# Kernel tuning notes

Measured on AMD Instinct MI355X. Metric: run time of the kernel, lower is better.

The kernel has to match this reference:

```python
import jax, jax.numpy as jnp
import numpy as np
import math

N_HEAD = 16

def setup_inputs() -> dict:
    key = jax.random.key(0)
    k1, k2, k3, k4, k5 = jax.random.split(key, 5)
    B, T, C = 8, 1024, 1024
    scale = 0.02
    return {
        "x": jax.random.normal(k1, (B, T, C), dtype=jnp.float32),
        "w_attn": jax.random.normal(k2, (C, 3 * C), dtype=jnp.float32) * scale,
        "b_attn": jax.random.normal(k3, (3 * C,), dtype=jnp.float32) * scale,
        "w_proj": jax.random.normal(k4, (C, C), dtype=jnp.float32) * scale,
        "b_proj": jax.random.normal(k5, (C,), dtype=jnp.float32) * scale,
    }

def reference(x, w_attn, b_attn, w_proj, b_proj):
    B, T, C = x.shape
    H = N_HEAD
    hd = C // H
    # QKV projection: [B,T,3C]
    qkv = jnp.einsum("btc,cd->btd", x, w_attn) + b_attn
    q, k, v = jnp.split(qkv, 3, axis=-1)
    # [B,T,C] -> [B,H,T,hd]
    def heads(t):
        return t.reshape(B, T, H, hd).transpose(0, 2, 1, 3)
    q, k, v = heads(q), heads(k), heads(v)
    # scaled QK^T: [B,H,T,T]
    att = jnp.einsum("bhqd,bhkd->bhqk", q, k) * (1.0 / math.sqrt(hd))
    # causal mask (tril of block_size cropped to T)
    causal = jnp.tril(jnp.ones((T, T), dtype=bool))
    att = jnp.where(causal, att, jnp.float32(-jnp.inf))
    att = jax.nn.softmax(att, axis=-1)
    # attention-weighted values: [B,H,T,hd] -> [B,T,C]
    y = jnp.einsum("bhqk,bhkd->bhqd", att, v)
    y = y.transpose(0, 2, 1, 3).reshape(B, T, C)
    # output projection
    return jnp.einsum("btc,cd->btd", y, w_proj) + b_proj
```

## Files before the change

kernel.cpp:

```cpp
#include <hip/hip_runtime.h>

typedef __bf16 bf16x8 __attribute__((ext_vector_type(8)));
typedef float f32x4 __attribute__((ext_vector_type(4)));
typedef unsigned short u16;
typedef unsigned int u32;
typedef unsigned long long u64;

__device__ __forceinline__ u16 f2bf(float f) {
  u32 u = __builtin_bit_cast(u32, f);
  u32 r = (u + 0x7FFFu + ((u >> 16) & 1u)) >> 16;
  return (u16)r;
}

__device__ __forceinline__ void gload_lds16(const u16* g, u16* l) {
  __builtin_amdgcn_global_load_lds(
      (const __attribute__((address_space(1))) u32*)g,
      (__attribute__((address_space(3))) u32*)l, 16, 0, 0);
}

__global__ void cast_x_kernel(const float* __restrict__ in, u16* __restrict__ out, int n4) {
  int i = blockIdx.x * blockDim.x + threadIdx.x;
  if (i >= n4) return;
  float4 v = ((const float4*)in)[i];
  uint2 o;
  o.x = (u32)f2bf(v.x) | ((u32)f2bf(v.y) << 16);
  o.y = (u32)f2bf(v.z) | ((u32)f2bf(v.w) << 16);
  ((uint2*)out)[i] = o;
}

__global__ void transpose_cast_kernel(const float* __restrict__ in, u16* __restrict__ out,
                                      int K, int N) {
  __shared__ float tile[32][33];
  int n0 = blockIdx.x * 32, k0 = blockIdx.y * 32;
  int tx = threadIdx.x & 31, ty = threadIdx.x >> 5;
#pragma unroll
  for (int i = 0; i < 32; i += 8)
    tile[ty + i][tx] = in[(size_t)(k0 + ty + i) * N + n0 + tx];
  __syncthreads();
#pragma unroll
  for (int i = 0; i < 32; i += 8)
    out[(size_t)(n0 + ty + i) * K + k0 + tx] = f2bf(tile[tx][ty + i]);
}

__global__ __launch_bounds__(512, 2) void gemm256qk(
    const u16* __restrict__ A, const u16* __restrict__ Bt,
    const float* __restrict__ bias, u16* __restrict__ out_q,
    int M, int N, int K) {
  __shared__ alignas(16) u16 lds[2][2][256 * 64];
  const int tiles_n = N >> 8;
  const int bid = blockIdx.x;
  const int cpx = (int)gridDim.x >> 3;
  const int swz = (bid & 7) * cpx + (bid >> 3);
  const int tm = swz / tiles_n, tn = swz % tiles_n;
  const int tid = threadIdx.x, lane = tid & 63;
  const int w = tid >> 6, wm = w >> 2, wn = w & 3;
  const int lr = lane & 15, lg = lane >> 4;
  const int NT = K >> 6;

  f32x4 acc[2][2][4][2] = {};

  auto stage = [&](int t, int which) {
    const int isB = which & 1, half = which >> 1;
    const u16* mat = isB ? Bt : A;
    const int row0 = (isB ? tn : tm) * 256 + half * 128;
    u16* lbase = &lds[t & 1][isB][half * 8192];
#pragma unroll
    for (int j = 0; j < 2; ++j) {
      int c = tid + j * 512;
      int k8 = (c & 7) ^ ((c >> 3) & 7);
      int row = c >> 3;
      gload_lds16(mat + (size_t)(row0 + row) * K + t * 64 + k8 * 8, lbase + c * 8);
    }
  };
  auto rdA = [&](int cur, int mh, int m, int kk) -> bf16x8 {
    int row = mh * 128 + wm * 64 + m * 16 + lr;
    int e = (row * 64 + kk * 32 + lg * 8) ^ ((row & 7) << 3);
    return *(const bf16x8*)&lds[cur][0][e];
  };
  auto rdB = [&](int cur, int nh, int n, int kk) -> bf16x8 {
    int row = nh * 128 + wn * 32 + n * 16 + lr;
    int e = (row * 64 + kk * 32 + lg * 8) ^ ((row & 7) << 3);
    return *(const bf16x8*)&lds[cur][1][e];
  };

  stage(0, 0); stage(0, 1); stage(0, 2); stage(0, 3);
  stage(1, 0); stage(1, 1); stage(1, 2);
  asm volatile("s_waitcnt vmcnt(6)" ::: "memory");
  __builtin_amdgcn_s_barrier();

  bf16x8 af[4][2], b0[2][2], b1[2][2];
  for (int t = 0; t < NT; ++t) {
    const int cur = t & 1;
#pragma unroll
    for (int m = 0; m < 4; ++m)
#pragma unroll
      for (int kk = 0; kk < 2; ++kk) af[m][kk] = rdA(cur, 0, m, kk);
#pragma unroll
    for (int n = 0; n < 2; ++n)
#pragma unroll
      for (int kk = 0; kk < 2; ++kk) b0[n][kk] = rdB(cur, 0, n, kk);
    if (t + 1 < NT) stage(t + 1, 3);
    __builtin_amdgcn_s_barrier();
    asm volatile("s_waitcnt lgkmcnt(0)" ::: "memory");
    __builtin_amdgcn_s_setprio(1);
#pragma unroll
    for (int m = 0; m < 4; ++m)
#pragma unroll
      for (int n = 0; n < 2; ++n)
#pragma unroll
        for (int kk = 0; kk < 2; ++kk)
          acc[0][0][m][n] = __builtin_amdgcn_mfma_f32_16x16x32_bf16(b0[n][kk], af[m][kk], acc[0][0][m][n], 0, 0, 0);
    __builtin_amdgcn_s_setprio(0);
    __builtin_amdgcn_s_barrier();
#pragma unroll
    for (int n = 0; n < 2; ++n)
#pragma unroll
      for (int kk = 0; kk < 2; ++kk) b1[n][kk] = rdB(cur, 1, n, kk);
    if (t + 2 < NT) stage(t + 2, 0);
    __builtin_amdgcn_s_barrier();
    asm volatile("s_waitcnt lgkmcnt(0)" ::: "memory");
    __builtin_amdgcn_s_setprio(1);
#pragma unroll
    for (int m = 0; m < 4; ++m)
#pragma unroll
      for (int n = 0; n < 2; ++n)
#pragma unroll
        for (int kk = 0; kk < 2; ++kk)
          acc[0][1][m][n] = __builtin_amdgcn_mfma_f32_16x16x32_bf16(b1[n][kk], af[m][kk], acc[0][1][m][n], 0, 0, 0);
    __builtin_amdgcn_s_setprio(0);
    __builtin_amdgcn_s_barrier();
#pragma unroll
    for (int m = 0; m < 4; ++m)
#pragma unroll
      for (int kk = 0; kk < 2; ++kk) af[m][kk] = rdA(cur, 1, m, kk);
    if (t + 2 < NT) stage(t + 2, 1);
    __builtin_amdgcn_s_barrier();
    asm volatile("s_waitcnt lgkmcnt(0)" ::: "memory");
    __builtin_amdgcn_s_setprio(1);
#pragma unroll
    for (int m = 0; m < 4; ++m)
#pragma unroll
      for (int n = 0; n < 2; ++n)
#pragma unroll
        for (int kk = 0; kk < 2; ++kk)
          acc[1][0][m][n] = __builtin_amdgcn_mfma_f32_16x16x32_bf16(b0[n][kk], af[m][kk], acc[1][0][m][n], 0, 0, 0);
    __builtin_amdgcn_s_setprio(0);
    __builtin_amdgcn_s_barrier();
    if (t + 2 < NT) stage(t + 2, 2);
    __builtin_amdgcn_s_barrier();
    __builtin_amdgcn_s_setprio(1);
#pragma unroll
    for (int m = 0; m < 4; ++m)
#pragma unroll
      for (int n = 0; n < 2; ++n)
#pragma unroll
        for (int kk = 0; kk < 2; ++kk)
          acc[1][1][m][n] = __builtin_amdgcn_mfma_f32_16x16x32_bf16(b1[n][kk], af[m][kk], acc[1][1][m][n], 0, 0, 0);
    __builtin_amdgcn_s_setprio(0);
    if (t + 2 < NT) {
      asm volatile("s_waitcnt vmcnt(6)" ::: "memory");
    } else {
      asm volatile("s_waitcnt vmcnt(0)" ::: "memory");
    }
    __builtin_amdgcn_s_barrier();
  }

#pragma unroll
  for (int mh = 0; mh < 2; ++mh)
#pragma unroll
    for (int nh = 0; nh < 2; ++nh)
#pragma unroll
      for (int n = 0; n < 2; ++n) {
        int ncol = tn * 256 + nh * 128 + wn * 32 + n * 16 + lg * 4;
        float4 bv = *(const float4*)&bias[ncol];
        int which = ncol >> 10, c = ncol & 1023;
        int h = c >> 6, d = c & 63;
#pragma unroll
        for (int m = 0; m < 4; ++m) {
          int tok = tm * 256 + mh * 128 + wm * 64 + m * 16 + lr;
          int b = tok >> 10, t = tok & 1023;
          union { u16 s[4]; uint2 v; } pk;
          pk.s[0] = f2bf(acc[mh][nh][m][n][0] + bv.x);
          pk.s[1] = f2bf(acc[mh][nh][m][n][1] + bv.y);
          pk.s[2] = f2bf(acc[mh][nh][m][n][2] + bv.z);
          pk.s[3] = f2bf(acc[mh][nh][m][n][3] + bv.w);
          *(uint2*)&out_q[(size_t)which * 8388608 + ((((size_t)b * 16 + h) * 1024 + t) << 6) + d] = pk.v;
        }
      }
}

template <int MODE>
__global__ __launch_bounds__(256, 3) void gemm_bf16(
    const u16* __restrict__ A, const u16* __restrict__ Bt,
    const float* __restrict__ bias, u16* __restrict__ out_q,
    float* __restrict__ out_f, int M, int N, int K) {
  __shared__ alignas(16) u16 As[128 * 64];
  __shared__ alignas(16) u16 Bs[128 * 64];
  const int tiles_n = N >> 7;
  const int bid0 = blockIdx.x;
  const int cpx = (int)gridDim.x >> 3;
  const int swz = (bid0 & 7) * cpx + (bid0 >> 3);
  const int tm = swz / tiles_n;
  const int tn = swz % tiles_n;
  const int tid = threadIdx.x;
  const int wave = tid >> 6, lane = tid & 63;
  const int wr = (wave >> 1) * 64, wc = (wave & 1) * 64;
  const int lr = lane & 15, lg = lane >> 4;

  f32x4 acc[4][4] = {};
  const size_t a_base = (size_t)(tm * 128) * K;
  const size_t b_base = (size_t)(tn * 128) * K;

  for (int k0 = 0; k0 < K; k0 += 64) {
#pragma unroll
    for (int i = 0; i < 4; ++i) {
      int c = i * 256 + tid;
      int row = c >> 3, ch = c & 7;
      int sw = (ch ^ (row & 7)) * 8;
      gload_lds16(A + a_base + (size_t)row * K + k0 + sw, &As[c * 8]);
      gload_lds16(Bt + b_base + (size_t)row * K + k0 + sw, &Bs[c * 8]);
    }
    __syncthreads();
    bf16x8 af[4][2], bfr[4][2];
#pragma unroll
    for (int m = 0; m < 4; ++m) {
      int row = wr + m * 16 + lr;
#pragma unroll
      for (int kk = 0; kk < 2; ++kk)
        af[m][kk] = *(const bf16x8*)&As[(row * 64 + kk * 32 + lg * 8) ^ ((row & 7) << 3)];
    }
#pragma unroll
    for (int n = 0; n < 4; ++n) {
      int row = wc + n * 16 + lr;
#pragma unroll
      for (int kk = 0; kk < 2; ++kk)
        bfr[n][kk] = *(const bf16x8*)&Bs[(row * 64 + kk * 32 + lg * 8) ^ ((row & 7) << 3)];
    }
#pragma unroll
    for (int m = 0; m < 4; ++m)
#pragma unroll
      for (int n = 0; n < 4; ++n) {
        acc[m][n] = __builtin_amdgcn_mfma_f32_16x16x32_bf16(af[m][0], bfr[n][0], acc[m][n], 0, 0, 0);
        acc[m][n] = __builtin_amdgcn_mfma_f32_16x16x32_bf16(af[m][1], bfr[n][1], acc[m][n], 0, 0, 0);
      }
    __syncthreads();
  }

  if constexpr (MODE == 2) {
    const int tok0 = tm * 128 + wr;
    const int col0 = tn * 128 + wc;
#pragma unroll
    for (int n = 0; n < 4; ++n) {
      int ncol = col0 + n * 16 + lr;
      float bv = bias[ncol];
      int h = ncol >> 6, d = ncol & 63;
#pragma unroll
      for (int m = 0; m < 4; ++m) {
        int t0 = tok0 + m * 16 + lg * 4;
        int b = t0 >> 10, t = t0 & 1023;
        union { u16 s[4]; uint2 v; } pk;
        pk.s[0] = f2bf(acc[m][n][0] + bv);
        pk.s[1] = f2bf(acc[m][n][1] + bv);
        pk.s[2] = f2bf(acc[m][n][2] + bv);
        pk.s[3] = f2bf(acc[m][n][3] + bv);
        *(uint2*)&out_q[(((size_t)b * 16 + h) * 64 + d) * 1024 + t] = pk.v;
      }
    }
  } else {
    const int row0 = tm * 128 + wr;
    const int col0 = tn * 128 + wc;
#pragma unroll
    for (int n = 0; n < 4; ++n) {
      int col = col0 + n * 16 + lr;
      float bv = bias[col];
#pragma unroll
      for (int m = 0; m < 4; ++m)
#pragma unroll
        for (int r = 0; r < 4; ++r) {
          int mrow = row0 + m * 16 + lg * 4 + r;
          out_f[(size_t)mrow * N + col] = acc[m][n][r] + bv;
        }
    }
  }
}

__global__ __launch_bounds__(256, 2) void attn_kernel(
    const u16* __restrict__ Qb, const u16* __restrict__ Kb,
    const u16* __restrict__ Vb, u16* __restrict__ yb) {
  __shared__ alignas(16) u16 Ks[128 * 64];
  __shared__ alignas(16) u16 Vt[64 * 128];
  __shared__ alignas(16) u16 Pl[4][32 * 64];

  const int bid = blockIdx.x;
  const int xcd = bid & 7, j = bid >> 3;
  const int bh = ((j >> 2) << 3) + xcd;
  const int pr = j & 3;
  const size_t hb = (size_t)bh * 65536;
  const int tid = threadIdx.x, w = tid >> 6, lane = tid & 63;
  const int lr = lane & 15, lg = lane >> 4;
  const int b = bh >> 4, h = bh & 15;
  const float C2 = 0.18033688011112042f;

  for (int pass = 0; pass < 2; ++pass) {
    const int qt = pass ? (7 - pr) : pr;
    const int q0 = qt * 128 + w * 32;

    bf16x8 qf[2][2];
#pragma unroll
    for (int mi = 0; mi < 2; ++mi)
#pragma unroll
      for (int ks = 0; ks < 2; ++ks)
        qf[mi][ks] = *(const bf16x8*)&Qb[hb + (size_t)(q0 + mi * 16 + lr) * 64 + ks * 32 + lg * 8];

    float l_run[2] = {0.f, 0.f};
    f32x4 o[2][4] = {};

    const int nkt = qt + 1;
    for (int kt = 0; kt < nkt; ++kt) {
#pragma unroll
      for (int i = 0; i < 4; ++i) {
        int c = i * 256 + tid;
        int row = c >> 3, ch = c & 7;
        gload_lds16(Kb + hb + (size_t)(kt * 128 + row) * 64 + ((ch ^ (row & 7)) * 8), &Ks[c * 8]);
      }
#pragma unroll
      for (int i = 0; i < 4; ++i) {
        int c = i * 256 + tid;
        int row = c >> 4, ch = c & 15;
        gload_lds16(Vb + hb + (size_t)row * 1024 + kt * 128 + ((ch ^ (row & 15)) * 8), &Vt[c * 8]);
      }
      __syncthreads();

      f32x4 s[8][2] = {};
      __builtin_amdgcn_s_setprio(1);
#pragma unroll
      for (int ni = 0; ni < 8; ++ni) {
        int krow = ni * 16 + lr;
        bf16x8 kf0 = *(const bf16x8*)&Ks[(krow * 64 + lg * 8) ^ ((krow & 7) << 3)];
        bf16x8 kf1 = *(const bf16x8*)&Ks[(krow * 64 + 32 + lg * 8) ^ ((krow & 7) << 3)];
#pragma unroll
        for (int mi = 0; mi < 2; ++mi) {
          s[ni][mi] = __builtin_amdgcn_mfma_f32_16x16x32_bf16(kf0, qf[mi][0], s[ni][mi], 0, 0, 0);
          s[ni][mi] = __builtin_amdgcn_mfma_f32_16x16x32_bf16(kf1, qf[mi][1], s[ni][mi], 0, 0, 0);
        }
      }
      __builtin_amdgcn_s_setprio(0);

      const bool need_mask = (kt == qt);
#pragma unroll
      for (int mi = 0; mi < 2; ++mi) {
        if (need_mask) {
#pragma unroll
          for (int ni = 0; ni < 8; ++ni)
#pragma unroll
            for (int r = 0; r < 4; ++r) {
              int ka = kt * 128 + ni * 16 + lg * 4 + r;
              int qa = q0 + mi * 16 + lr;
              if (ka > qa) s[ni][mi][r] = -1e30f;
            }
        }
        float ps[8];
#pragma unroll
        for (int ni = 0; ni < 8; ++ni) {
#pragma unroll
          for (int r = 0; r < 4; ++r)
            s[ni][mi][r] = __builtin_amdgcn_exp2f(s[ni][mi][r] * C2);
          ps[ni] = (s[ni][mi][0] + s[ni][mi][1]) + (s[ni][mi][2] + s[ni][mi][3]);
        }
        l_run[mi] += ((ps[0] + ps[1]) + (ps[2] + ps[3])) + ((ps[4] + ps[5]) + (ps[6] + ps[7]));
      }
#pragma unroll
      for (int hh = 0; hh < 2; ++hh) {
#pragma unroll
        for (int mi = 0; mi < 2; ++mi) {
          int qrow = mi * 16 + lr;
          int sw = (qrow & 7) << 3;
#pragma unroll
          for (int nq = 0; nq < 4; ++nq) {
            int ni = hh * 4 + nq;
            u32 plo, phi;
            asm("v_cvt_pk_bf16_f32 %0, %1, %2" : "=v"(plo) : "v"(s[ni][mi][0]), "v"(s[ni][mi][1]));
            asm("v_cvt_pk_bf16_f32 %0, %1, %2" : "=v"(phi) : "v"(s[ni][mi][2]), "v"(s[ni][mi][3]));
            u64 pv = (u64)plo | ((u64)phi << 32);
            int e = (qrow * 64 + nq * 16 + lg * 4) ^ sw;
            *(u64*)&Pl[w][e] = pv;
          }
        }
        asm volatile("s_waitcnt lgkmcnt(0)" ::: "memory");
        __builtin_amdgcn_s_setprio(1);
#pragma unroll
        for (int kh = 0; kh < 2; ++kh) {
          int ksl = hh * 2 + kh;
          bf16x8 pf[2];
#pragma unroll
          for (int mi = 0; mi < 2; ++mi) {
            int prow = mi * 16 + lr;
            pf[mi] = *(const bf16x8*)&Pl[w][(prow * 64 + kh * 32 + lg * 8) ^ ((prow & 7) << 3)];
          }
#pragma unroll
          for (int nd = 0; nd < 4; ++nd) {
            int vrow = nd * 16 + lr;
            bf16x8 vf = *(const bf16x8*)&Vt[(vrow * 128 + ksl * 32 + lg * 8) ^ ((vrow & 15) << 3)];
#pragma unroll
            for (int mi = 0; mi < 2; ++mi)
              o[mi][nd] = __builtin_amdgcn_mfma_f32_16x16x32_bf16(pf[mi], vf, o[mi][nd], 0, 0, 0);
          }
        }
        __builtin_amdgcn_s_setprio(0);
      }
      __syncthreads();
    }

#pragma unroll
    for (int mi = 0; mi < 2; ++mi) {
      float lt = l_run[mi];
      lt += __shfl_xor(lt, 16);
      lt += __shfl_xor(lt, 32);
      f32x4 inv;
#pragma unroll
      for (int r = 0; r < 4; ++r) inv[r] = 1.f / __shfl(lt, lg * 4 + r);
#pragma unroll
      for (int nd = 0; nd < 4; ++nd)
#pragma unroll
        for (int r = 0; r < 4; ++r) {
          int t = q0 + mi * 16 + lg * 4 + r;
          int c = h * 64 + nd * 16 + lr;
          yb[((size_t)b * 1024 + t) * 1024 + c] = f2bf(o[mi][nd][r] * inv[r]);
        }
    }
    __syncthreads();
  }
}

extern "C" void kernel_launch(void* const* d_in, const int* in_sizes, int n_in,
                              void* d_out, int out_size, void* d_ws, size_t ws_size,
                              hipStream_t stream) {
  const float* x = (const float*)d_in[0];
  const float* w_attn = (const float*)d_in[1];
  const float* b_attn = (const float*)d_in[2];
  const float* w_proj = (const float*)d_in[3];
  const float* b_proj = (const float*)d_in[4];
  float* out = (float*)d_out;

  u16* ws = (u16*)d_ws;
  u16* xb = ws;
  u16* watT = xb + 8388608;
  u16* wpT = watT + 3145728;
  u16* Qb = wpT + 1048576;
  u16* Vt = Qb + 2 * 8388608;
  u16* yb = xb;

  cast_x_kernel<<<8192, 256, 0, stream>>>(x, xb, 2097152);
  {
    dim3 g(96, 32);
    transpose_cast_kernel<<<g, 256, 0, stream>>>(w_attn, watT, 1024, 3072);
  }
  {
    dim3 g(32, 32);
    transpose_cast_kernel<<<g, 256, 0, stream>>>(w_proj, wpT, 1024, 1024);
  }
  gemm256qk<<<256, 512, 0, stream>>>(xb, watT, b_attn, Qb, 8192, 2048, 1024);
  gemm_bf16<2><<<64 * 8, 256, 0, stream>>>(xb, watT + (size_t)2048 * 1024, b_attn + 2048, Vt,
                                           nullptr, 8192, 1024, 1024);
  attn_kernel<<<512, 256, 0, stream>>>(Qb, Qb + 8388608, Vt, yb);
  gemm_bf16<1><<<64 * 8, 256, 0, stream>>>(yb, wpT, b_proj, nullptr, out, 8192, 1024, 1024);
}
```

Baseline: 138.8 us.

## Share K/V tile loads between paired causal query tiles in one pass

The attention kernel previously ran two sequential passes per block, one for the low query tile and one for the mirrored high tile, and loaded K/V tiles into LDS separately for each. Now a single loop over key tiles loads each K/V tile once and applies it to both query streams, with the low stream active only up to its diagonal. This roughly halves LDS fill traffic and barriers for the low tile. In exchange it keeps two sets of Q fragments and output accumulators live, which raises register pressure under launch_bounds(256,2) and may cause spills or lower occupancy.

```diff
diff --git a/kernel.cpp b/kernel.cpp
--- a/kernel.cpp
+++ b/kernel.cpp
@@ -301,116 +301,128 @@
   const int b = bh >> 4, h = bh & 15;
   const float C2 = 0.18033688011112042f;
 
-  for (int pass = 0; pass < 2; ++pass) {
-    const int qt = pass ? (7 - pr) : pr;
-    const int q0 = qt * 128 + w * 32;
-
-    bf16x8 qf[2][2];
-#pragma unroll
-    for (int mi = 0; mi < 2; ++mi)
-#pragma unroll
-      for (int ks = 0; ks < 2; ++ks)
-        qf[mi][ks] = *(const bf16x8*)&Qb[hb + (size_t)(q0 + mi * 16 + lr) * 64 + ks * 32 + lg * 8];
-
-    float l_run[2] = {0.f, 0.f};
-    f32x4 o[2][4] = {};
-
-    const int nkt = qt + 1;
-    for (int kt = 0; kt < nkt; ++kt) {
-#pragma unroll
-      for (int i = 0; i < 4; ++i) {
-        int c = i * 256 + tid;
-        int row = c >> 3, ch = c & 7;
-        gload_lds16(Kb + hb + (size_t)(kt * 128 + row) * 64 + ((ch ^ (row & 7)) * 8), &Ks[c * 8]);
-      }
-#pragma unroll
-      for (int i = 0; i < 4; ++i) {
-        int c = i * 256 + tid;
-        int row = c >> 4, ch = c & 15;
-        gload_lds16(Vb + hb + (size_t)row * 1024 + kt * 128 + ((ch ^ (row & 15)) * 8), &Vt[c * 8]);
-      }
-      __syncthreads();
-
-      f32x4 s[8][2] = {};
+  const int qtL = pr, qtH = 7 - pr;
+  const int q0L = qtL * 128 + w * 32, q0H = qtH * 128 + w * 32;
+
+  bf16x8 qfL[2][2], qfH[2][2];
+#pragma unroll
+  for (int mi = 0; mi < 2; ++mi)
+#pragma unroll
+    for (int ks = 0; ks < 2; ++ks) {
+      qfL[mi][ks] = *(const bf16x8*)&Qb[hb + (size_t)(q0L + mi * 16 + lr) * 64 + ks * 32 + lg * 8];
+      qfH[mi][ks] = *(const bf16x8*)&Qb[hb + (size_t)(q0H + mi * 16 + lr) * 64 + ks * 32 + lg * 8];
+    }
+
+  float lL[2] = {0.f, 0.f}, lH[2] = {0.f, 0.f};
+  f32x4 oL[2][4] = {}, oH[2][4] = {};
+
+  auto run_stream = [&](const bf16x8 (&qf)[2][2], f32x4 (&o)[2][4], float (&l_run)[2],
+                        int qt, int q0, int kt) {
+    f32x4 s[8][2] = {};
+    __builtin_amdgcn_s_setprio(1);
+#pragma unroll
+    for (int ni = 0; ni < 8; ++ni) {
+      int krow = ni * 16 + lr;
+      bf16x8 kf0 = *(const bf16x8*)&Ks[(krow * 64 + lg * 8) ^ ((krow & 7) << 3)];
+      bf16x8 kf1 = *(const bf16x8*)&Ks[(krow * 64 + 32 + lg * 8) ^ ((krow & 7) << 3)];
+#pragma unroll
+      for (int mi = 0; mi < 2; ++mi) {
+        s[ni][mi] = __builtin_amdgcn_mfma_f32_16x16x32_bf16(kf0, qf[mi][0], s[ni][mi], 0, 0, 0);
+        s[ni][mi] = __builtin_amdgcn_mfma_f32_16x16x32_bf16(kf1, qf[mi][1], s[ni][mi], 0, 0, 0);
+      }
+    }
+    __builtin_amdgcn_s_setprio(0);
+
+    const bool need_mask = (kt == qt);
+#pragma unroll
+    for (int mi = 0; mi < 2; ++mi) {
+      if (need_mask) {
+#pragma unroll
+        for (int ni = 0; ni < 8; ++ni)
+#pragma unroll
+          for (int r = 0; r < 4; ++r) {
+            int ka = kt * 128 + ni * 16 + lg * 4 + r;
+            int qa = q0 + mi * 16 + lr;
+            if (ka > qa) s[ni][mi][r] = -1e30f;
+          }
+      }
+      float ps[8];
+#pragma unroll
+      for (int ni = 0; ni < 8; ++ni) {
+#pragma unroll
+        for (int r = 0; r < 4; ++r)
+          s[ni][mi][r] = __builtin_amdgcn_exp2f(s[ni][mi][r] * C2);
+        ps[ni] = (s[ni][mi][0] + s[ni][mi][1]) + (s[ni][mi][2] + s[ni][mi][3]);
+      }
+      l_run[mi] += ((ps[0] + ps[1]) + (ps[2] + ps[3])) + ((ps[4] + ps[5]) + (ps[6] + ps[7]));
+    }
+#pragma unroll
+    for (int hh = 0; hh < 2; ++hh) {
+#pragma unroll
+      for (int mi = 0; mi < 2; ++mi) {
+        int qrow = mi * 16 + lr;
+        int sw = (qrow & 7) << 3;
+#pragma unroll
+        for (int nq = 0; nq < 4; ++nq) {
+          int ni = hh * 4 + nq;
+          u32 plo, phi;
+          asm("v_cvt_pk_bf16_f32 %0, %1, %2" : "=v"(plo) : "v"(s[ni][mi][0]), "v"(s[ni][mi][1]));
+          asm("v_cvt_pk_bf16_f32 %0, %1, %2" : "=v"(phi) : "v"(s[ni][mi][2]), "v"(s[ni][mi][3]));
+          u64 pv = (u64)plo | ((u64)phi << 32);
+          int e = (qrow * 64 + nq * 16 + lg * 4) ^ sw;
+          *(u64*)&Pl[w][e] = pv;
+        }
+      }
+      asm volatile("s_waitcnt lgkmcnt(0)" ::: "memory");
       __builtin_amdgcn_s_setprio(1);
 #pragma unroll
-      for (int ni = 0; ni < 8; ++ni) {
-        int krow = ni * 16 + lr;
-        bf16x8 kf0 = *(const bf16x8*)&Ks[(krow * 64 + lg * 8) ^ ((krow & 7) << 3)];
-        bf16x8 kf1 = *(const bf16x8*)&Ks[(krow * 64 + 32 + lg * 8) ^ ((krow & 7) << 3)];
+      for (int kh = 0; kh < 2; ++kh) {
+        int ksl = hh * 2 + kh;
+        bf16x8 pf[2];
 #pragma unroll
         for (int mi = 0; mi < 2; ++mi) {
-          s[ni][mi] = __builtin_amdgcn_mfma_f32_16x16x32_bf16(kf0, qf[mi][0], s[ni][mi], 0, 0, 0);
-          s[ni][mi] = __builtin_amdgcn_mfma_f32_16x16x32_bf16(kf1, qf[mi][1], s[ni][mi], 0, 0, 0);
+          int prow = mi * 16 + lr;
+          pf[mi] = *(const bf16x8*)&Pl[w][(prow * 64 + kh * 32 + lg * 8) ^ ((prow & 7) << 3)];
+        }
+#pragma unroll
+        for (int nd = 0; nd < 4; ++nd) {
+          int vrow = nd * 16 + lr;
+          bf16x8 vf = *(const bf16x8*)&Vt[(vrow * 128 + ksl * 32 + lg * 8) ^ ((vrow & 15) << 3)];
+#pragma unroll
+          for (int mi = 0; mi < 2; ++mi)
+            o[mi][nd] = __builtin_amdgcn_mfma_f32_16x16x32_bf16(pf[mi], vf, o[mi][nd], 0, 0, 0);
         }
       }
       __builtin_amdgcn_s_setprio(0);
-
-      const bool need_mask = (kt == qt);
-#pragma unroll
-      for (int mi = 0; mi < 2; ++mi) {
-        if (need_mask) {
-#pragma unroll
-          for (int ni = 0; ni < 8; ++ni)
-#pragma unroll
-            for (int r = 0; r < 4; ++r) {
-              int ka = kt * 128 + ni * 16 + lg * 4 + r;
-              int qa = q0 + mi * 16 + lr;
-              if (ka > qa) s[ni][mi][r] = -1e30f;
-            }
-        }
-        float ps[8];
-#pragma unroll
-        for (int ni = 0; ni < 8; ++ni) {
-#pragma unroll
-          for (int r = 0; r < 4; ++r)
-            s[ni][mi][r] = __builtin_amdgcn_exp2f(s[ni][mi][r] * C2);
-          ps[ni] = (s[ni][mi][0] + s[ni][mi][1]) + (s[ni][mi][2] + s[ni][mi][3]);
-        }
-        l_run[mi] += ((ps[0] + ps[1]) + (ps[2] + ps[3])) + ((ps[4] + ps[5]) + (ps[6] + ps[7]));
-      }
-#pragma unroll
-      for (int hh = 0; hh < 2; ++hh) {
-#pragma unroll
-        for (int mi = 0; mi < 2; ++mi) {
-          int qrow = mi * 16 + lr;
-          int sw = (qrow & 7) << 3;
-#pragma unroll
-          for (int nq = 0; nq < 4; ++nq) {
-            int ni = hh * 4 + nq;
-            u32 plo, phi;
-            asm("v_cvt_pk_bf16_f32 %0, %1, %2" : "=v"(plo) : "v"(s[ni][mi][0]), "v"(s[ni][mi][1]));
-            asm("v_cvt_pk_bf16_f32 %0, %1, %2" : "=v"(phi) : "v"(s[ni][mi][2]), "v"(s[ni][mi][3]));
-            u64 pv = (u64)plo | ((u64)phi << 32);
-            int e = (qrow * 64 + nq * 16 + lg * 4) ^ sw;
-            *(u64*)&Pl[w][e] = pv;
-          }
-        }
-        asm volatile("s_waitcnt lgkmcnt(0)" ::: "memory");
-        __builtin_amdgcn_s_setprio(1);
-#pragma unroll
-        for (int kh = 0; kh < 2; ++kh) {
-          int ksl = hh * 2 + kh;
-          bf16x8 pf[2];
-#pragma unroll
-          for (int mi = 0; mi < 2; ++mi) {
-            int prow = mi * 16 + lr;
-            pf[mi] = *(const bf16x8*)&Pl[w][(prow * 64 + kh * 32 + lg * 8) ^ ((prow & 7) << 3)];
-          }
-#pragma unroll
-          for (int nd = 0; nd < 4; ++nd) {
-            int vrow = nd * 16 + lr;
-            bf16x8 vf = *(const bf16x8*)&Vt[(vrow * 128 + ksl * 32 + lg * 8) ^ ((vrow & 15) << 3)];
-#pragma unroll
-            for (int mi = 0; mi < 2; ++mi)
-              o[mi][nd] = __builtin_amdgcn_mfma_f32_16x16x32_bf16(pf[mi], vf, o[mi][nd], 0, 0, 0);
-          }
-        }
-        __builtin_amdgcn_s_setprio(0);
-      }
-      __syncthreads();
-    }
-
+    }
+  };
+
+  const int nkt = qtH + 1;
+  for (int kt = 0; kt < nkt; ++kt) {
+#pragma unroll
+    for (int i = 0; i < 4; ++i) {
+      int c = i * 256 + tid;
+      int row = c >> 3, ch = c & 7;
+      gload_lds16(Kb + hb + (size_t)(kt * 128 + row) * 64 + ((ch ^ (row & 7)) * 8), &Ks[c * 8]);
+    }
+#pragma unroll
+    for (int i = 0; i < 4; ++i) {
+      int c = i * 256 + tid;
+      int row = c >> 4, ch = c & 15;
+      gload_lds16(Vb + hb + (size_t)row * 1024 + kt * 128 + ((ch ^ (row & 15)) * 8), &Vt[c * 8]);
+    }
+    __syncthreads();
+
+    run_stream(qfH, oH, lH, qtH, q0H, kt);
+    if (kt <= qtL) run_stream(qfL, oL, lL, qtL, q0L, kt);
+    __syncthreads();
+  }
+
+#pragma unroll
+  for (int st = 0; st < 2; ++st) {
+    f32x4 (&o)[2][4] = st ? oH : oL;
+    float* l_run = st ? lH : lL;
+    int q0 = st ? q0H : q0L;
 #pragma unroll
     for (int mi = 0; mi < 2; ++mi) {
       float lt = l_run[mi];
@@ -428,7 +440,6 @@
           yb[((size_t)b * 1024 + t) * 1024 + c] = f2bf(o[mi][nd][r] * inv[r]);
         }
     }
-    __syncthreads();
   }
 }
 
```

New measurement: 196.7 us. 1.42x slower.
